# Kernel optimization log

Measured on AMD Instinct MI355X. Metric: run time of the kernel, lower is better.

## Reference

```python
import jax, jax.numpy as jnp
import numpy as np

B, L, E, H = 4, 1024, 1024, 16
DH = E // H
EPS = 1e-5


def _linear(x, W, b):
    # torch nn.Linear: x @ W.T + b, W: (out, in)
    return jnp.einsum('ble,oe->blo', x, W) + b


def _layernorm(x, g, b):
    m = jnp.mean(x, axis=-1, keepdims=True)
    v = jnp.var(x, axis=-1, keepdims=True)
    return (x - m) * jax.lax.rsqrt(v + EPS) * g + b


def setup_inputs() -> dict:
    key = jax.random.key(0)
    ks = jax.random.split(key, 16)
    s = 1.0 / np.sqrt(E)
    inp = {
        'x': jax.random.normal(ks[0], (B, L, E), dtype=jnp.float32),
        'mask': jax.random.randint(ks[1], (B, L), 0, 2, dtype=jnp.int32),
        'Wq': jax.random.uniform(ks[2], (E, E), jnp.float32, -s, s),
        'bq': jax.random.uniform(ks[3], (E,), jnp.float32, -s, s),
        'Wk': jax.random.uniform(ks[4], (E, E), jnp.float32, -s, s),
        'bk': jax.random.uniform(ks[5], (E,), jnp.float32, -s, s),
        'Wv': jax.random.uniform(ks[6], (E, E), jnp.float32, -s, s),
        'bv': jax.random.uniform(ks[7], (E,), jnp.float32, -s, s),
        'Wo': jax.random.uniform(ks[8], (E, E), jnp.float32, -s, s),
        'bo': jax.random.uniform(ks[9], (E,), jnp.float32, -s, s),
        'g1': jnp.ones((E,), jnp.float32),
        'b1': jnp.zeros((E,), jnp.float32),
        'Wf': jax.random.uniform(ks[10], (E, E), jnp.float32, -s, s),
        'bf': jax.random.uniform(ks[11], (E,), jnp.float32, -s, s),
        'g2': jnp.ones((E,), jnp.float32),
        'b2': jnp.zeros((E,), jnp.float32),
        'alpha': jnp.float32(0.5),
    }
    return inp


def reference(x, mask, Wq, bq, Wk, bk, Wv, bv, Wo, bo, g1, b1, Wf, bf, g2, b2, alpha):
    q = _linear(x, Wq, bq)
    k = _linear(x, Wk, bk)
    v = _linear(x, Wv, bv)
    # Faithful to source: reshape(B, H, L, -1) with NO transpose (non-standard head split)
    q = q.reshape(B, H, L, DH)
    k = k.reshape(B, H, L, DH)
    v = v.reshape(B, H, L, DH)
    scores = jnp.einsum('bhqd,bhkd->bhqk', q, k) / np.sqrt(DH).astype(np.float32)
    # mask (B,L) -> (B,1,1,L), fill -1e10 where mask == 0
    m = mask[:, None, None, :]
    scores = jnp.where(m == 0, jnp.float32(-1e10), scores)
    attn = jax.nn.softmax(scores, axis=-1)
    att = jnp.einsum('bhqk,bhkd->bhqd', attn, v)  # (B,H,L,DH)
    att = att.transpose(0, 2, 1, 3).reshape(B, L, E)
    att = _linear(att, Wo, bo)
    # dropout is identity in eval mode
    skip1 = _layernorm(x + att, g1, b1)
    fcc = jax.nn.gelu(_linear(skip1, Wf, bf), approximate=False)
    skip2 = _layernorm(skip1 + fcc, g2, b2)
    return x * alpha + skip2 * (1.0 - alpha)
```

## Files before the change

kernel.cpp:

```cpp
#include <hip/hip_runtime.h>
#include <hip/hip_bf16.h>
#include <string.h>

typedef __attribute__((ext_vector_type(8))) short short8;
typedef __attribute__((ext_vector_type(4))) float f32x4;
typedef __attribute__((ext_vector_type(4))) unsigned short u16x4;

#define MFMA_BF16(a, b, c) __builtin_amdgcn_mfma_f32_16x16x32_bf16((a), (b), (c), 0, 0, 0)

__device__ __forceinline__ unsigned short f2bf(float f) {
  unsigned int u = __builtin_bit_cast(unsigned int, f);
  u += 0x7fffu + ((u >> 16) & 1u);
  return (unsigned short)(u >> 16);
}

__device__ __forceinline__ float bf2f(unsigned short s) {
  unsigned int u = ((unsigned int)s) << 16;
  return __builtin_bit_cast(float, u);
}

__device__ __forceinline__ unsigned pk_bf16(float a, float b) {
  __hip_bfloat162 h = __float22bfloat162_rn(float2{a, b});
  unsigned r;
  memcpy(&r, &h, 4);
  return r;
}

__device__ __forceinline__ void gload_lds16(const void* g, void* lds) {
  __builtin_amdgcn_global_load_lds(
      (const __attribute__((address_space(1))) unsigned int*)g,
      (__attribute__((address_space(3))) unsigned int*)lds, 16, 0, 0);
}

__global__ __launch_bounds__(256) void cast_all(const float* __restrict__ x,
                                                const float* __restrict__ Wq,
                                                const float* __restrict__ Wk,
                                                const float* __restrict__ Wv,
                                                const float* __restrict__ Wo,
                                                const float* __restrict__ Wf,
                                                unsigned short* __restrict__ xb,
                                                unsigned short* __restrict__ Wqkv,
                                                unsigned short* __restrict__ Wob,
                                                unsigned short* __restrict__ Wfb,
                                                const int* __restrict__ mask,
                                                const float* __restrict__ bq,
                                                const float* __restrict__ bk,
                                                const float* __restrict__ bv,
                                                float* __restrict__ ma,
                                                float* __restrict__ bcat) {
  int i = blockIdx.x * 256 + threadIdx.x;
  if (i < 2359296) {
    const float* src;
    unsigned short* dst;
    int j;
    if (i < 1048576)      { src = x;  dst = xb;             j = i; }
    else if (i < 1310720) { src = Wq; dst = Wqkv;           j = i - 1048576; }
    else if (i < 1572864) { src = Wk; dst = Wqkv + 1048576; j = i - 1310720; }
    else if (i < 1835008) { src = Wv; dst = Wqkv + 2097152; j = i - 1572864; }
    else if (i < 2097152) { src = Wo; dst = Wob;            j = i - 1835008; }
    else                  { src = Wf; dst = Wfb;            j = i - 2097152; }
    float4 v = ((const float4*)src)[j];
    u16x4 r = { f2bf(v.x), f2bf(v.y), f2bf(v.z), f2bf(v.w) };
    ((u16x4*)dst)[j] = r;
  } else {
    int j = i - 2359296;
    if (j < 4096) ma[j] = (mask[j] == 0) ? -1.4426950408889634e10f : 0.0f;
    int k = j - 4096;
    if (k >= 0 && k < 3072) {
      float v = (k < 1024) ? bq[k] : (k < 2048 ? bk[k - 1024] : bv[k - 2048]);
      bcat[k] = v;
    }
  }
}

template <int EPI>
__global__ __launch_bounds__(256) void gemm_lds64(const unsigned short* __restrict__ A,
                                                  const unsigned short* __restrict__ W,
                                                  const float* __restrict__ bias,
                                                  void* __restrict__ Cout,
                                                  int M, int N, int K) {
  __shared__ unsigned short At[2][128 * 64];
  __shared__ unsigned short Bt[2][64 * 64];

  const int tid = threadIdx.x;
  const int w = tid >> 6, l = tid & 63;
  const int lr = l & 15, lq = l >> 4;
  const int row0 = blockIdx.x * 128;
  const int col0 = blockIdx.y * 64;

  const int sr8 = l >> 3;
  const int sc8 = ((l & 7) ^ (l >> 3)) * 8;

  const int NT = K >> 6;

#define GSTAGE(s, t)                                                              \
  {                                                                               \
    const int kt_ = (t) * 64;                                                     \
    _Pragma("unroll")                                                             \
    for (int j = 0; j < 4; j++) {                                                 \
      const int r_ = (w * 4 + j) * 8 + sr8;                                       \
      gload_lds16(A + (size_t)(row0 + r_) * K + kt_ + sc8, &At[s][(w * 4 + j) * 512]); \
    }                                                                             \
    _Pragma("unroll")                                                             \
    for (int j = 0; j < 2; j++) {                                                 \
      const int r_ = (w * 2 + j) * 8 + sr8;                                       \
      gload_lds16(W + (size_t)(col0 + r_) * K + kt_ + sc8, &Bt[s][(w * 2 + j) * 512]); \
    }                                                                             \
  }

  GSTAGE(0, 0);
  GSTAGE(1, 1);
  asm volatile("s_waitcnt vmcnt(6)" ::: "memory");
  __builtin_amdgcn_s_barrier();
  __builtin_amdgcn_sched_barrier(0);

  f32x4 acc[2][4] = {};

#pragma unroll 1
  for (int t = 0; t < NT; t++) {
    const int cur = t & 1;

    short8 af[2][2], bfr[2][4];
#pragma unroll
    for (int ks = 0; ks < 2; ks++) {
      const int slot = ((ks * 4 + lq) ^ (lr & 7)) * 8;
#pragma unroll
      for (int m = 0; m < 2; m++)
        af[ks][m] = *(const short8*)&At[cur][(w * 32 + m * 16 + lr) * 64 + slot];
#pragma unroll
      for (int n = 0; n < 4; n++)
        bfr[ks][n] = *(const short8*)&Bt[cur][(n * 16 + lr) * 64 + slot];
    }
    asm volatile("s_waitcnt lgkmcnt(0)" ::: "memory");
    __builtin_amdgcn_s_barrier();
    __builtin_amdgcn_sched_barrier(0);

    if (t + 2 < NT) GSTAGE(cur, t + 2);

    __builtin_amdgcn_s_setprio(1);
#pragma unroll
    for (int ks = 0; ks < 2; ks++)
#pragma unroll
      for (int m = 0; m < 2; m++)
#pragma unroll
        for (int n = 0; n < 4; n++)
          acc[m][n] = MFMA_BF16(af[ks][m], bfr[ks][n], acc[m][n]);
    __builtin_amdgcn_s_setprio(0);

    if (t + 2 < NT) {
      asm volatile("s_waitcnt vmcnt(6)" ::: "memory");
      __builtin_amdgcn_s_barrier();
      __builtin_amdgcn_sched_barrier(0);
    } else if (t + 2 == NT) {
      asm volatile("s_waitcnt vmcnt(0)" ::: "memory");
      __builtin_amdgcn_s_barrier();
      __builtin_amdgcn_sched_barrier(0);
    }
  }
#undef GSTAGE

#pragma unroll
  for (int n = 0; n < 4; n++) {
    const int col = col0 + n * 16 + lr;
    const float bv = bias[col];
#pragma unroll
    for (int m = 0; m < 2; m++) {
      const int row = row0 + w * 32 + m * 16 + lq * 4;
#pragma unroll
      for (int r = 0; r < 4; r++) {
        float v = acc[m][n][r] + bv;
        if (EPI == 0) {
          ((unsigned short*)Cout)[(size_t)(row + r) * N + col] = f2bf(v);
        } else {
          float g = 0.5f * v * (1.0f + erff(v * 0.70710678118654752f));
          ((unsigned short*)Cout)[(size_t)(row + r) * N + col] = f2bf(g);
        }
      }
    }
  }
}

__global__ __launch_bounds__(256) void vtrans_kernel(const unsigned short* __restrict__ qkv,
                                                     unsigned short* __restrict__ VT) {
  const int bh = blockIdx.x;
  const int kt = blockIdx.y;
  const int t = threadIdx.x;
  const int d = t & 63, kg = t >> 6;
  const unsigned short* basev =
      qkv + ((size_t)(bh >> 4) * 1024 + (bh & 15) * 64) * 3072 + 2048;
  const unsigned short* src = basev + (size_t)(kt * 4 + kg) * 3072 + d;
  unsigned short vals[16];
#pragma unroll
  for (int j = 0; j < 16; j++) vals[j] = src[j * 64];
  short8 v0, v1;
#pragma unroll
  for (int j = 0; j < 8; j++) { v0[j] = (short)vals[j]; v1[j] = (short)vals[8 + j]; }
  size_t dst = ((size_t)bh * 64 + d) * 1024 + kt * 64 + kg * 16;
  *(short8*)&VT[dst] = v0;
  *(short8*)&VT[dst + 8] = v1;
}

__global__ __launch_bounds__(256) void attn14_kernel(const unsigned short* __restrict__ qkv,
                                                     const unsigned short* __restrict__ VT,
                                                     const float* __restrict__ maskadd,
                                                     unsigned short* __restrict__ att) {
  __shared__ unsigned short Kt[3][2048];
  __shared__ unsigned short Vt[3][2048];
  __shared__ float ma_lds[1024];
  __shared__ unsigned short Pl[4][640];

  const int bh = blockIdx.x, b = bh >> 4, h = bh & 15;
  const int qb = blockIdx.y;
  const int tid = threadIdx.x, w = tid >> 6, l = tid & 63;
  const int lr = l & 15, lq = l >> 4;

  const unsigned short* baseq = qkv + ((size_t)b * 1024 + h * 64) * 3072;
  const unsigned short* basek = baseq + 1024;
  const unsigned short* vtb = VT + (size_t)bh * 64 * 1024;

  const int skey = (tid >> 2) & 31;
  const int skd = (tid >> 7) * 32 + (((tid & 3) ^ ((skey >> 1) & 3)) * 8);
  const int svd = tid >> 2;
  const int svc = ((tid & 3) ^ ((svd >> 1) & 3)) * 8;

  short8 qf[2];
  const int q0 = qb * 64 + w * 16;
  {
    const int p = q0 + lr;
    const unsigned short* qa = baseq + (p >> 4) * 3072 + (p & 15) * 64;
    qf[0] = *(const short8*)(qa + lq * 8);
    qf[1] = *(const short8*)(qa + 32 + lq * 8);
  }
  ((float4*)ma_lds)[tid] = ((const float4*)(maskadd + b * 1024))[tid];

#pragma unroll
  for (int t0 = 0; t0 < 2; t0++) {
    const int pk = t0 * 32 + skey;
    gload_lds16(basek + (pk >> 4) * 3072 + (pk & 15) * 64 + skd, (char*)&Kt[t0][0] + w * 1024);
    gload_lds16(vtb + (size_t)svd * 1024 + t0 * 32 + svc, (char*)&Vt[t0][0] + w * 1024);
  }
  asm volatile("s_waitcnt lgkmcnt(0) vmcnt(2)" ::: "memory");
  __builtin_amdgcn_s_barrier();
  __builtin_amdgcn_sched_barrier(0);

  float ll = 0.f;
  f32x4 o[4] = {};
  unsigned short* pw = &Pl[w][0];
  constexpr float SC = 0.18033688011112042f;
  const int cx = (lq ^ ((lr >> 1) & 3)) * 8;

#pragma unroll 1
  for (int kt = 0; kt < 32; kt++) {
    const int cur = kt % 3;
    if (kt < 30) {
      const int st = (kt + 2) % 3;
      const int pk = (kt + 2) * 32 + skey;
      gload_lds16(basek + (pk >> 4) * 3072 + (pk & 15) * 64 + skd,
                  (char*)&Kt[st][0] + w * 1024);
      gload_lds16(vtb + (size_t)svd * 1024 + (kt + 2) * 32 + svc,
                  (char*)&Vt[st][0] + w * 1024);
    }

    const unsigned short* KtL = &Kt[cur][0];
    const unsigned short* VtL = &Vt[cur][0];
    short8 vf[4];
#pragma unroll
    for (int n = 0; n < 4; n++)
      vf[n] = *(const short8*)&VtL[(n * 16 + lr) * 32 + cx];

    const float4 mk0 = *(const float4*)&ma_lds[kt * 32 + lq * 4];
    const float4 mk1 = *(const float4*)&ma_lds[kt * 32 + 16 + lq * 4];

    short8 kf00 = *(const short8*)&KtL[lr * 32 + cx];
    short8 kf01 = *(const short8*)&KtL[1024 + lr * 32 + cx];
    short8 kf10 = *(const short8*)&KtL[(16 + lr) * 32 + cx];
    short8 kf11 = *(const short8*)&KtL[1024 + (16 + lr) * 32 + cx];
    f32x4 s0 = {0.f, 0.f, 0.f, 0.f}, s1 = {0.f, 0.f, 0.f, 0.f};
    __builtin_amdgcn_s_setprio(1);
    s0 = MFMA_BF16(kf00, qf[0], s0);
    s0 = MFMA_BF16(kf01, qf[1], s0);
    s1 = MFMA_BF16(kf10, qf[0], s1);
    s1 = MFMA_BF16(kf11, qf[1], s1);
    __builtin_amdgcn_s_setprio(0);

    float p[8], rs = 0.f;
#pragma unroll
    for (int r = 0; r < 4; r++) {
      p[r]     = __builtin_amdgcn_exp2f(s0[r] * SC + ((const float*)&mk0)[r]);
      p[4 + r] = __builtin_amdgcn_exp2f(s1[r] * SC + ((const float*)&mk1)[r]);
    }
#pragma unroll
    for (int i = 0; i < 8; i++) rs += p[i];
    ll += rs;

    uint2 wa, wb;
    wa.x = pk_bf16(p[0], p[1]);
    wa.y = pk_bf16(p[2], p[3]);
    wb.x = pk_bf16(p[4], p[5]);
    wb.y = pk_bf16(p[6], p[7]);
    *(uint2*)&pw[lr * 40 + lq * 4] = wa;
    *(uint2*)&pw[lr * 40 + 16 + lq * 4] = wb;

    asm volatile("s_waitcnt lgkmcnt(0)" ::: "memory");
    const short8 pa = *(const short8*)&pw[lr * 40 + lq * 8];
    __builtin_amdgcn_s_setprio(1);
#pragma unroll
    for (int n = 0; n < 4; n++)
      o[n] = MFMA_BF16(pa, vf[n], o[n]);
    __builtin_amdgcn_s_setprio(0);

    if (kt < 30) {
      asm volatile("s_waitcnt vmcnt(2)" ::: "memory");
      __builtin_amdgcn_s_barrier();
      __builtin_amdgcn_sched_barrier(0);
    } else if (kt == 30) {
      asm volatile("s_waitcnt vmcnt(0)" ::: "memory");
      __builtin_amdgcn_s_barrier();
      __builtin_amdgcn_sched_barrier(0);
    }
  }

  float lf = ll;
  lf += __shfl_xor(lf, 16);
  lf += __shfl_xor(lf, 32);
  float inv[4];
#pragma unroll
  for (int r = 0; r < 4; r++) inv[r] = 1.0f / __shfl(lf, lq * 4 + r);
#pragma unroll
  for (int r = 0; r < 4; r++) {
    const int q = q0 + lq * 4 + r;
    const size_t obase = ((size_t)b * 1024 + q) * 1024 + h * 64;
#pragma unroll
    for (int n = 0; n < 4; n++)
      att[obase + n * 16 + lr] = f2bf(o[n][r] * inv[r]);
  }
}

__global__ __launch_bounds__(256) void ln1_kernel(const float* __restrict__ x,
                                                  const unsigned short* __restrict__ attp,
                                                  const float* __restrict__ g,
                                                  const float* __restrict__ bt,
                                                  unsigned short* __restrict__ sb) {
  const int row = blockIdx.x, tid = threadIdx.x;
  float4 xv = ((const float4*)(x + row * 1024))[tid];
  u16x4 ab = ((const u16x4*)(attp + row * 1024))[tid];
  float4 v = {xv.x + bf2f(ab[0]), xv.y + bf2f(ab[1]), xv.z + bf2f(ab[2]), xv.w + bf2f(ab[3])};
  float s = v.x + v.y + v.z + v.w;
  float sq = v.x * v.x + v.y * v.y + v.z * v.z + v.w * v.w;
#pragma unroll
  for (int off = 1; off < 64; off <<= 1) { s += __shfl_xor(s, off); sq += __shfl_xor(sq, off); }
  __shared__ float ws[8];
  int wv = tid >> 6, l = tid & 63;
  if (l == 0) { ws[wv] = s; ws[4 + wv] = sq; }
  __syncthreads();
  s = ws[0] + ws[1] + ws[2] + ws[3];
  sq = ws[4] + ws[5] + ws[6] + ws[7];
  float mean = s * (1.0f / 1024.0f);
  float var = sq * (1.0f / 1024.0f) - mean * mean;
  float rs = rsqrtf(var + 1e-5f);
  float4 gv = ((const float4*)g)[tid];
  float4 bv = ((const float4*)bt)[tid];
  u16x4 yb = { f2bf((v.x - mean) * rs * gv.x + bv.x),
               f2bf((v.y - mean) * rs * gv.y + bv.y),
               f2bf((v.z - mean) * rs * gv.z + bv.z),
               f2bf((v.w - mean) * rs * gv.w + bv.w) };
  ((u16x4*)(sb + row * 1024))[tid] = yb;
}

__global__ __launch_bounds__(256) void ln2_kernel(const unsigned short* __restrict__ skip,
                                                  const unsigned short* __restrict__ fcc,
                                                  const float* __restrict__ g,
                                                  const float* __restrict__ bt,
                                                  const float* __restrict__ x,
                                                  const float* __restrict__ alphap,
                                                  float* __restrict__ out) {
  const int row = blockIdx.x, tid = threadIdx.x;
  u16x4 sb = ((const u16x4*)(skip + row * 1024))[tid];
  u16x4 fb = ((const u16x4*)(fcc + row * 1024))[tid];
  float4 v = {bf2f(sb[0]) + bf2f(fb[0]), bf2f(sb[1]) + bf2f(fb[1]),
              bf2f(sb[2]) + bf2f(fb[2]), bf2f(sb[3]) + bf2f(fb[3])};
  float s = v.x + v.y + v.z + v.w;
  float sq = v.x * v.x + v.y * v.y + v.z * v.z + v.w * v.w;
#pragma unroll
  for (int off = 1; off < 64; off <<= 1) { s += __shfl_xor(s, off); sq += __shfl_xor(sq, off); }
  __shared__ float ws[8];
  int wv = tid >> 6, l = tid & 63;
  if (l == 0) { ws[wv] = s; ws[4 + wv] = sq; }
  __syncthreads();
  s = ws[0] + ws[1] + ws[2] + ws[3];
  sq = ws[4] + ws[5] + ws[6] + ws[7];
  float mean = s * (1.0f / 1024.0f);
  float var = sq * (1.0f / 1024.0f) - mean * mean;
  float rs = rsqrtf(var + 1e-5f);
  float4 gv = ((const float4*)g)[tid];
  float4 bv = ((const float4*)bt)[tid];
  float alpha = alphap[0];
  float beta = 1.0f - alpha;
  float4 xv = ((const float4*)(x + row * 1024))[tid];
  float4 y;
  y.x = xv.x * alpha + ((v.x - mean) * rs * gv.x + bv.x) * beta;
  y.y = xv.y * alpha + ((v.y - mean) * rs * gv.y + bv.y) * beta;
  y.z = xv.z * alpha + ((v.z - mean) * rs * gv.z + bv.z) * beta;
  y.w = xv.w * alpha + ((v.w - mean) * rs * gv.w + bv.w) * beta;
  ((float4*)(out + row * 1024))[tid] = y;
}

extern "C" void kernel_launch(void* const* d_in, const int* in_sizes, int n_in,
                              void* d_out, int out_size, void* d_ws, size_t ws_size,
                              hipStream_t stream) {
  const float* x  = (const float*)d_in[0];
  const int* mask = (const int*)d_in[1];
  const float* Wq = (const float*)d_in[2];
  const float* bq = (const float*)d_in[3];
  const float* Wk = (const float*)d_in[4];
  const float* bk = (const float*)d_in[5];
  const float* Wv = (const float*)d_in[6];
  const float* bv = (const float*)d_in[7];
  const float* Wo = (const float*)d_in[8];
  const float* bo = (const float*)d_in[9];
  const float* g1 = (const float*)d_in[10];
  const float* b1 = (const float*)d_in[11];
  const float* Wf = (const float*)d_in[12];
  const float* bf = (const float*)d_in[13];
  const float* g2 = (const float*)d_in[14];
  const float* b2 = (const float*)d_in[15];
  const float* alpha = (const float*)d_in[16];
  float* out = (float*)d_out;

  char* ws = (char*)d_ws;
  size_t off = 0;
  unsigned short* xb   = (unsigned short*)(ws + off); off += 8388608;
  unsigned short* Wqkv = (unsigned short*)(ws + off); off += 6291456;
  unsigned short* Wob  = (unsigned short*)(ws + off); off += 2097152;
  unsigned short* Wfb  = (unsigned short*)(ws + off); off += 2097152;
  float* bcat          = (float*)(ws + off);          off += 12288;
  float* maf           = (float*)(ws + off);          off += 16384;
  unsigned short* qkvb = (unsigned short*)(ws + off); off += 25165824;
  unsigned short* attb = (unsigned short*)(ws + off); off += 8388608;
  float* tmp           = (float*)(ws + off);          off += 16777216;
  unsigned short* s1b  = (unsigned short*)(ws + off); off += 8388608;

  unsigned short* VT  = (unsigned short*)tmp;
  unsigned short* obf = (unsigned short*)tmp;
  unsigned short* fbf = (unsigned short*)tmp + 4194304;

  cast_all<<<9244, 256, 0, stream>>>(x, Wq, Wk, Wv, Wo, Wf, xb, Wqkv, Wob, Wfb,
                                     mask, bq, bk, bv, maf, bcat);

  gemm_lds64<0><<<dim3(32, 48), 256, 0, stream>>>(xb, Wqkv, bcat, qkvb, 4096, 3072, 1024);

  vtrans_kernel<<<dim3(64, 16), 256, 0, stream>>>(qkvb, VT);

  attn14_kernel<<<dim3(64, 16), 256, 0, stream>>>(qkvb, VT, maf, attb);

  gemm_lds64<0><<<dim3(32, 16), 256, 0, stream>>>(attb, Wob, bo, obf, 4096, 1024, 1024);

  ln1_kernel<<<4096, 256, 0, stream>>>(x, obf, g1, b1, s1b);

  gemm_lds64<3><<<dim3(32, 16), 256, 0, stream>>>(s1b, Wfb, bf, fbf, 4096, 1024, 1024);

  ln2_kernel<<<4096, 256, 0, stream>>>(s1b, fbf, g2, b2, x, alpha, out);
}
```

Before: 136.3 us.

## Process 64-key tiles per iteration with double buffering in attention

Restructures the attention loop to handle two 32-key sub-tiles per iteration (16 iterations instead of 32), with a 2-stage double buffer in place of the 3-stage ring. The aim is to halve the number of block barriers and waitcnt stalls per key sweep. In exchange, prefetch depth drops from two tiles ahead to one, and each iteration waits on vmcnt(0), so load latency is less hidden. Register pressure also rises because V fragments are held for both sub-tiles.

```diff
diff --git a/kernel.cpp b/kernel.cpp
--- a/kernel.cpp
+++ b/kernel.cpp
@@ -200,14 +200,14 @@
   *(short8*)&VT[dst + 8] = v1;
 }
 
-__global__ __launch_bounds__(256) void attn14_kernel(const unsigned short* __restrict__ qkv,
+__global__ __launch_bounds__(256) void attn15_kernel(const unsigned short* __restrict__ qkv,
                                                      const unsigned short* __restrict__ VT,
                                                      const float* __restrict__ maskadd,
                                                      unsigned short* __restrict__ att) {
-  __shared__ unsigned short Kt[3][2048];
-  __shared__ unsigned short Vt[3][2048];
+  __shared__ unsigned short Kt[2][2][2048];
+  __shared__ unsigned short Vt[2][2][2048];
   __shared__ float ma_lds[1024];
-  __shared__ unsigned short Pl[4][640];
+  __shared__ unsigned short Pl[4][2][640];
 
   const int bh = blockIdx.x, b = bh >> 4, h = bh & 15;
   const int qb = blockIdx.y;
@@ -234,86 +234,94 @@
   ((float4*)ma_lds)[tid] = ((const float4*)(maskadd + b * 1024))[tid];
 
 #pragma unroll
-  for (int t0 = 0; t0 < 2; t0++) {
-    const int pk = t0 * 32 + skey;
-    gload_lds16(basek + (pk >> 4) * 3072 + (pk & 15) * 64 + skd, (char*)&Kt[t0][0] + w * 1024);
-    gload_lds16(vtb + (size_t)svd * 1024 + t0 * 32 + svc, (char*)&Vt[t0][0] + w * 1024);
-  }
-  asm volatile("s_waitcnt lgkmcnt(0) vmcnt(2)" ::: "memory");
+  for (int sub = 0; sub < 2; sub++) {
+    const int pk = sub * 32 + skey;
+    gload_lds16(basek + (pk >> 4) * 3072 + (pk & 15) * 64 + skd,
+                (char*)&Kt[0][sub][0] + w * 1024);
+    gload_lds16(vtb + (size_t)svd * 1024 + sub * 32 + svc,
+                (char*)&Vt[0][sub][0] + w * 1024);
+  }
+  asm volatile("s_waitcnt lgkmcnt(0) vmcnt(0)" ::: "memory");
   __builtin_amdgcn_s_barrier();
   __builtin_amdgcn_sched_barrier(0);
 
   float ll = 0.f;
   f32x4 o[4] = {};
-  unsigned short* pw = &Pl[w][0];
+  unsigned short* pws[2] = {&Pl[w][0][0], &Pl[w][1][0]};
   constexpr float SC = 0.18033688011112042f;
   const int cx = (lq ^ ((lr >> 1) & 3)) * 8;
 
 #pragma unroll 1
-  for (int kt = 0; kt < 32; kt++) {
-    const int cur = kt % 3;
-    if (kt < 30) {
-      const int st = (kt + 2) % 3;
-      const int pk = (kt + 2) * 32 + skey;
-      gload_lds16(basek + (pk >> 4) * 3072 + (pk & 15) * 64 + skd,
-                  (char*)&Kt[st][0] + w * 1024);
-      gload_lds16(vtb + (size_t)svd * 1024 + (kt + 2) * 32 + svc,
-                  (char*)&Vt[st][0] + w * 1024);
-    }
-
-    const unsigned short* KtL = &Kt[cur][0];
-    const unsigned short* VtL = &Vt[cur][0];
-    short8 vf[4];
-#pragma unroll
-    for (int n = 0; n < 4; n++)
-      vf[n] = *(const short8*)&VtL[(n * 16 + lr) * 32 + cx];
-
-    const float4 mk0 = *(const float4*)&ma_lds[kt * 32 + lq * 4];
-    const float4 mk1 = *(const float4*)&ma_lds[kt * 32 + 16 + lq * 4];
-
-    short8 kf00 = *(const short8*)&KtL[lr * 32 + cx];
-    short8 kf01 = *(const short8*)&KtL[1024 + lr * 32 + cx];
-    short8 kf10 = *(const short8*)&KtL[(16 + lr) * 32 + cx];
-    short8 kf11 = *(const short8*)&KtL[1024 + (16 + lr) * 32 + cx];
-    f32x4 s0 = {0.f, 0.f, 0.f, 0.f}, s1 = {0.f, 0.f, 0.f, 0.f};
-    __builtin_amdgcn_s_setprio(1);
-    s0 = MFMA_BF16(kf00, qf[0], s0);
-    s0 = MFMA_BF16(kf01, qf[1], s0);
-    s1 = MFMA_BF16(kf10, qf[0], s1);
-    s1 = MFMA_BF16(kf11, qf[1], s1);
-    __builtin_amdgcn_s_setprio(0);
-
-    float p[8], rs = 0.f;
-#pragma unroll
-    for (int r = 0; r < 4; r++) {
-      p[r]     = __builtin_amdgcn_exp2f(s0[r] * SC + ((const float*)&mk0)[r]);
-      p[4 + r] = __builtin_amdgcn_exp2f(s1[r] * SC + ((const float*)&mk1)[r]);
-    }
-#pragma unroll
-    for (int i = 0; i < 8; i++) rs += p[i];
-    ll += rs;
-
-    uint2 wa, wb;
-    wa.x = pk_bf16(p[0], p[1]);
-    wa.y = pk_bf16(p[2], p[3]);
-    wb.x = pk_bf16(p[4], p[5]);
-    wb.y = pk_bf16(p[6], p[7]);
-    *(uint2*)&pw[lr * 40 + lq * 4] = wa;
-    *(uint2*)&pw[lr * 40 + 16 + lq * 4] = wb;
+  for (int t = 0; t < 16; t++) {
+    const int cur = t & 1;
+    if (t < 15) {
+      const int ns = cur ^ 1;
+#pragma unroll
+      for (int sub = 0; sub < 2; sub++) {
+        const int pk = (t + 1) * 64 + sub * 32 + skey;
+        gload_lds16(basek + (pk >> 4) * 3072 + (pk & 15) * 64 + skd,
+                    (char*)&Kt[ns][sub][0] + w * 1024);
+        gload_lds16(vtb + (size_t)svd * 1024 + (t + 1) * 64 + sub * 32 + svc,
+                    (char*)&Vt[ns][sub][0] + w * 1024);
+      }
+    }
+
+    short8 vf[2][4];
+#pragma unroll
+    for (int sub = 0; sub < 2; sub++) {
+      const unsigned short* KtL = &Kt[cur][sub][0];
+      const unsigned short* VtL = &Vt[cur][sub][0];
+#pragma unroll
+      for (int n = 0; n < 4; n++)
+        vf[sub][n] = *(const short8*)&VtL[(n * 16 + lr) * 32 + cx];
+
+      const int kb = t * 64 + sub * 32;
+      const float4 mk0 = *(const float4*)&ma_lds[kb + lq * 4];
+      const float4 mk1 = *(const float4*)&ma_lds[kb + 16 + lq * 4];
+
+      short8 kf00 = *(const short8*)&KtL[lr * 32 + cx];
+      short8 kf01 = *(const short8*)&KtL[1024 + lr * 32 + cx];
+      short8 kf10 = *(const short8*)&KtL[(16 + lr) * 32 + cx];
+      short8 kf11 = *(const short8*)&KtL[1024 + (16 + lr) * 32 + cx];
+      f32x4 s0 = {0.f, 0.f, 0.f, 0.f}, s1 = {0.f, 0.f, 0.f, 0.f};
+      __builtin_amdgcn_s_setprio(1);
+      s0 = MFMA_BF16(kf00, qf[0], s0);
+      s0 = MFMA_BF16(kf01, qf[1], s0);
+      s1 = MFMA_BF16(kf10, qf[0], s1);
+      s1 = MFMA_BF16(kf11, qf[1], s1);
+      __builtin_amdgcn_s_setprio(0);
+
+      float p[8], rs = 0.f;
+#pragma unroll
+      for (int r = 0; r < 4; r++) {
+        p[r]     = __builtin_amdgcn_exp2f(s0[r] * SC + ((const float*)&mk0)[r]);
+        p[4 + r] = __builtin_amdgcn_exp2f(s1[r] * SC + ((const float*)&mk1)[r]);
+      }
+#pragma unroll
+      for (int i = 0; i < 8; i++) rs += p[i];
+      ll += rs;
+
+      uint2 wa, wb;
+      wa.x = pk_bf16(p[0], p[1]);
+      wa.y = pk_bf16(p[2], p[3]);
+      wb.x = pk_bf16(p[4], p[5]);
+      wb.y = pk_bf16(p[6], p[7]);
+      *(uint2*)&pws[sub][lr * 40 + lq * 4] = wa;
+      *(uint2*)&pws[sub][lr * 40 + 16 + lq * 4] = wb;
+    }
 
     asm volatile("s_waitcnt lgkmcnt(0)" ::: "memory");
-    const short8 pa = *(const short8*)&pw[lr * 40 + lq * 8];
-    __builtin_amdgcn_s_setprio(1);
-#pragma unroll
-    for (int n = 0; n < 4; n++)
-      o[n] = MFMA_BF16(pa, vf[n], o[n]);
-    __builtin_amdgcn_s_setprio(0);
-
-    if (kt < 30) {
-      asm volatile("s_waitcnt vmcnt(2)" ::: "memory");
-      __builtin_amdgcn_s_barrier();
-      __builtin_amdgcn_sched_barrier(0);
-    } else if (kt == 30) {
+#pragma unroll
+    for (int sub = 0; sub < 2; sub++) {
+      const short8 pa = *(const short8*)&pws[sub][lr * 40 + lq * 8];
+      __builtin_amdgcn_s_setprio(1);
+#pragma unroll
+      for (int n = 0; n < 4; n++)
+        o[n] = MFMA_BF16(pa, vf[sub][n], o[n]);
+      __builtin_amdgcn_s_setprio(0);
+    }
+
+    if (t < 15) {
       asm volatile("s_waitcnt vmcnt(0)" ::: "memory");
       __builtin_amdgcn_s_barrier();
       __builtin_amdgcn_sched_barrier(0);
@@ -451,7 +459,7 @@
 
   vtrans_kernel<<<dim3(64, 16), 256, 0, stream>>>(qkvb, VT);
 
-  attn14_kernel<<<dim3(64, 16), 256, 0, stream>>>(qkvb, VT, maf, attb);
+  attn15_kernel<<<dim3(64, 16), 256, 0, stream>>>(qkvb, VT, maf, attb);
 
   gemm_lds64<0><<<dim3(32, 16), 256, 0, stream>>>(attb, Wob, bo, obf, 4096, 1024, 1024);
 
```

New measurement: 143.9 us. +5.5%, slower.
